# Kernel tuning notes

Measured on AMD Instinct MI355X. Metric: run time of the kernel, lower is better.

Reference implementation:

```python
import jax, jax.numpy as jnp
import numpy as np
from jax import lax

NB_DIGITS = 2
BASE = 10
NUMS = BASE ** NB_DIGITS            # 100 possible values per number
SUMS = 2 * (NUMS - 1) + 1           # 199 possible sums (circuit roots)
B = 4096                            # logical batch size
N_IMAGES = B * 2 * NB_DIGITS        # 16384 digit images


def setup_inputs() -> dict:
    key = jax.random.key(0)
    ks = jax.random.split(key, 11)
    s = 0.1
    return {
        "images": jax.random.normal(ks[0], (N_IMAGES, 1, 28, 28), jnp.float32),
        "conv1_w": jax.random.normal(ks[1], (6, 1, 5, 5), jnp.float32) * s,
        "conv1_b": jax.random.normal(ks[2], (6,), jnp.float32) * s,
        "conv2_w": jax.random.normal(ks[3], (16, 6, 5, 5), jnp.float32) * s,
        "conv2_b": jax.random.normal(ks[4], (16,), jnp.float32) * s,
        "fc1_w": jax.random.normal(ks[5], (120, 256), jnp.float32) * s,
        "fc1_b": jax.random.normal(ks[6], (120,), jnp.float32) * s,
        "fc2_w": jax.random.normal(ks[7], (84, 120), jnp.float32) * s,
        "fc2_b": jax.random.normal(ks[8], (84,), jnp.float32) * s,
        "fc3_w": jax.random.normal(ks[9], (10, 84), jnp.float32) * s,
        "fc3_b": jax.random.normal(ks[10], (10,), jnp.float32) * s,
    }


def _conv(x, w, b):
    y = lax.conv_general_dilated(x, w, (1, 1), 'VALID',
                                 dimension_numbers=('NCHW', 'OIHW', 'NCHW'))
    return y + b[None, :, None, None]


def _maxpool2(x):
    return lax.reduce_window(x, -jnp.inf, lax.max, (1, 1, 2, 2), (1, 1, 2, 2), 'VALID')


def _lenet(x, c1w, c1b, c2w, c2b, f1w, f1b, f2w, f2b, f3w, f3b):
    x = jax.nn.relu(_maxpool2(_conv(x, c1w, c1b)))   # [N,6,12,12]
    x = jax.nn.relu(_maxpool2(_conv(x, c2w, c2b)))   # [N,16,4,4]
    x = x.reshape(-1, 16 * 4 * 4)
    x = jax.nn.relu(x @ f1w.T + f1b)
    x = jax.nn.relu(x @ f2w.T + f2b)
    x = x @ f3w.T + f3b
    return jax.nn.log_softmax(x, axis=-1)            # [N,10]


def _circuit(lp):
    # lp: [B, 2*NB_DIGITS, 10] per-digit log-probs.
    # Vars layout from get_circuit: positions 0..NB_DIGITS-1 = n1 digits (MSB first),
    # positions NB_DIGITS..2*NB_DIGITS-1 = n2 digits. Neg-literal weights are 0 in
    # log space (the `zeros` arg), so each model's weight = sum of digit log-probs;
    # OR over models = logsumexp grouped by n1+n2.
    d = jnp.arange(NUMS)
    hi, lo = d // BASE, d % BASE
    lp1 = lp[:, 0, hi] + lp[:, 1, lo]                # [B, NUMS] log P(n1=k)
    lp2 = lp[:, 2, hi] + lp[:, 3, lo]                # [B, NUMS] log P(n2=k)
    M = (lp1[:, :, None] + lp2[:, None, :]).reshape(lp.shape[0], -1)  # [B, NUMS^2]
    seg = (jnp.arange(NUMS)[:, None] + jnp.arange(NUMS)[None, :]).reshape(-1)
    Mf = M.T                                          # [NUMS^2, B]
    m = jax.ops.segment_max(Mf, seg, num_segments=SUMS)              # [SUMS, B]
    ssum = jax.ops.segment_sum(jnp.exp(Mf - m[seg]), seg, num_segments=SUMS)
    return (jnp.log(ssum) + m).T                      # [B, SUMS] log P(sum=s)


def reference(images, conv1_w, conv1_b, conv2_w, conv2_b,
              fc1_w, fc1_b, fc2_w, fc2_b, fc3_w, fc3_b):
    logp = _lenet(images, conv1_w, conv1_b, conv2_w, conv2_b,
                  fc1_w, fc1_b, fc2_w, fc2_b, fc3_w, fc3_b)   # [N_IMAGES,10]
    lp = logp.reshape(B, 2 * NB_DIGITS, BASE)
    return _circuit(lp)
```

## Files before the change

kernel.cpp:

```cpp
#include <hip/hip_runtime.h>
#include <hip/hip_bf16.h>
#include <math.h>

#define SUMS 199
#define NBLK 1024

typedef __attribute__((ext_vector_type(8))) short short8;
typedef __attribute__((ext_vector_type(4))) float float4v;

union Frag8 { short8 v; unsigned u[4]; uint4 q; };

static __device__ inline unsigned pk_bf16(float a, float b) {
    __hip_bfloat162 h = __float22bfloat162_rn(make_float2(a, b));
    union { __hip_bfloat162 h; unsigned u; } c; c.h = h; return c.u;
}

__global__ __launch_bounds__(256) void convert_weights(
    const float* __restrict__ f1w, const float* __restrict__ f2w,
    const float* __restrict__ f3w, const float* __restrict__ c1w,
    const float* __restrict__ c2w, uint4* __restrict__ ws)
{
    const int g = blockIdx.x * 256 + threadIdx.x;
    if (g >= 6400) return;
    float v[8];
    if (g < 5824) {
        const float* W; int O, K, ld, nt, s, l;
        if (g < 4096)      { W = f1w; O = 120; K = 256; ld = 256; nt = g >> 9; s = (g >> 6) & 7; l = g & 63; }
        else if (g < 5632) { const int f = g - 4096; W = f2w; O = 84; K = 120; ld = 120; nt = f >> 8; s = (f >> 6) & 3; l = f & 63; }
        else               { const int f = g - 5632; W = f3w; O = 10; K = 84;  ld = 84;  nt = 0; s = f >> 6; l = f & 63; }
        const int o = nt * 16 + (l & 15);
        #pragma unroll
        for (int j = 0; j < 8; ++j) {
            const int k = 32 * s + 8 * (l >> 4) + j;
            v[j] = (o < O && k < K) ? W[o * ld + k] : 0.f;
        }
    } else if (g < 6336) {
        const int f = g - 5824, s = f >> 6, l = f & 63;
        const int c = l & 15, h = l >> 4;
        const int pos = 4 * s + h;
        const int ky = pos / 5, kx = pos % 5;
        const bool ok = (pos < 25);
        #pragma unroll
        for (int jp = 0; jp < 4; ++jp) {
            v[2 * jp]     = (ok && 2 * jp < 6)     ? c2w[c * 150 + (2 * jp) * 25 + ky * 5 + kx]     : 0.f;
            v[2 * jp + 1] = (ok && 2 * jp + 1 < 6) ? c2w[c * 150 + (2 * jp + 1) * 25 + ky * 5 + kx] : 0.f;
        }
    } else {
        const int l = (g - 6336) & 63;
        const int c = l & 15, h = l >> 4;
        const int oc = c >> 1, xs = c & 1;
        #pragma unroll
        for (int j = 0; j < 8; ++j) {
            const int p = h * 4 + (j >> 1);
            float w = 0.f;
            if (p < 15 && c < 12) {
                const int ky = p / 3, kx = 2 * (p % 3) + (j & 1) - xs;
                if (kx >= 0 && kx < 5) w = c1w[oc * 25 + ky * 5 + kx];
            }
            v[j] = w;
        }
    }
    uint4 r;
    r.x = pk_bf16(v[0], v[1]); r.y = pk_bf16(v[2], v[3]);
    r.z = pk_bf16(v[4], v[5]); r.w = pk_bf16(v[6], v[7]);
    ws[g] = r;
}

__global__ __launch_bounds__(256, 4) void lenet_circuit_kernel(
    const float* __restrict__ images,
    const float* __restrict__ c1b, const float* __restrict__ c2b,
    const float* __restrict__ f1b, const float* __restrict__ f2b,
    const float* __restrict__ f3b, const uint4* __restrict__ wsb,
    float* __restrict__ out)
{
    __shared__ __align__(16) unsigned char s_mem[39680];
    unsigned*       imgu = (unsigned*)s_mem;
    uint2*          imgw = (uint2*)s_mem;
    unsigned short* p1s  = (unsigned short*)(s_mem + 12672);
    const uint4*    p1u4 = (const uint4*)(s_mem + 12672);
    unsigned*       A1d  = (unsigned*)(s_mem + 31232);
    const uint4*    A1q  = (const uint4*)(s_mem + 31232);
    float*          pgf  = (float*)(s_mem + 7680);
    float*          Hf   = (float*)(s_mem + 8448);
    float*          Lf   = (float*)(s_mem + 8768);

    const int t = threadIdx.x, bid = blockIdx.x;
    const int lane = t & 63, wav = t >> 6;
    const int c = lane & 15, h = lane >> 4;
    const uint4 z4 = {0u, 0u, 0u, 0u};

    const int qxo = c >> 2, parity = (c >> 1) & 1, irel = c & 1;

    {
        uint4* pz = (uint4*)(s_mem + 12672) + 2 * wav * 145;
        for (int j = lane; j < 290; j += 64) pz[j] = z4;
    }
    Frag8 a1; a1.q = wsb[6336 + lane];
    Frag8 w2[7];
    #pragma unroll
    for (int s = 0; s < 7; ++s) w2[s].q = wsb[5824 + s * 64 + lane];
    int koff[7];
    #pragma unroll
    for (int s = 0; s < 7; ++s) {
        const int pos = 4 * s + h;
        koff[s] = (pos < 25) ? (pos / 5) * 12 + (pos % 5) : 0;
    }
    int pd[4];
    #pragma unroll
    for (int q = 0; q < 4; ++q) {
        const int p = 4 * h + q;
        pd[q] = (p < 15) ? (p / 3) * 14 + (p % 3) : 0;
    }
    float bias0 = 0.f, bias1 = 0.f;
    if (h < 3) { bias0 = c1b[2 * h]; bias1 = c1b[2 * h + 1]; }
    const float b2v = c2b[c];

    float4 pf[7];
    {
        const float4* g1 = (const float4*)(images + (size_t)bid * 12544 + 6272) + 392 * wav;
        #pragma unroll
        for (int k = 0; k < 7; ++k) {
            const int i = lane + 64 * k;
            if (i < 392) pf[k] = g1[i];
        }
    }

    auto do_stage1 = [&]() {
        #pragma unroll
        for (int k = 0; k < 7; ++k) {
            const int i = lane + 64 * k;
            if (i < 392) {
                const int im = 2 * wav + (i >= 196);
                const int j = i - ((i >= 196) ? 196 : 0);
                uint2 wv; wv.x = pk_bf16(pf[k].x, pf[k].y); wv.y = pk_bf16(pf[k].z, pf[k].w);
                imgw[im * 198 + j] = wv;
            }
        }
    };
    auto do_conv1 = [&]() {
        const int img = 2 * wav + irel;
        const int imb = img * 396 + parity * 14 + qxo;
        for (int qy = 0; qy < 12; ++qy) {
            #pragma unroll
            for (int qxg = 0; qxg < 3; ++qxg) {
                const int base = imb + qy * 28 + qxg * 4;
                Frag8 bf;
                #pragma unroll
                for (int q = 0; q < 4; ++q) bf.u[q] = imgu[base + pd[q]];
                float4v acc = {0.f, 0.f, 0.f, 0.f};
                acc = __builtin_amdgcn_mfma_f32_16x16x32_bf16(a1.v, bf.v, acc, 0, 0, 0);
                float v0 = fmaxf(acc[0], acc[1]);
                float v1 = fmaxf(acc[2], acc[3]);
                v0 = fmaxf(v0, __shfl_xor(v0, 2));
                v1 = fmaxf(v1, __shfl_xor(v1, 2));
                if (parity == 0 && h < 3) {
                    const int qx = qxg * 4 + qxo;
                    *(unsigned*)&p1s[img * 1160 + qy * 96 + qx * 8 + 2 * h] =
                        pk_bf16(fmaxf(v0 + bias0, 0.f), fmaxf(v1 + bias1, 0.f));
                }
            }
        }
    };
    auto do_conv2 = [&](int pass) {
        const int pxl = (c & 1) + 2 * ((c >> 2) & 1);
        const int pyl = ((c >> 1) & 1) + 2 * ((c >> 3) & 1);
        #pragma unroll
        for (int ii = 0; ii < 2; ++ii) {
            const int i0 = 2 * wav + ii;
            #pragma unroll
            for (int mt = 0; mt < 4; ++mt) {
                const int px = pxl + 4 * (mt & 1), py = pyl + 4 * (mt >> 1);
                const int base = i0 * 145 + py * 12 + px;
                float4v acc = {0.f, 0.f, 0.f, 0.f};
                #pragma unroll
                for (int s = 0; s < 7; ++s) {
                    Frag8 af; af.q = p1u4[base + koff[s]];
                    acc = __builtin_amdgcn_mfma_f32_16x16x32_bf16(af.v, w2[s].v, acc, 0, 0, 0);
                }
                const float p = fmaxf(fmaxf(acc[0], acc[1]), fmaxf(acc[2], acc[3]));
                float v = fmaxf(p + b2v, 0.f);
                const float vp = __shfl_xor(v, 16);
                if ((h & 1) == 0) {
                    const int qy = (h >> 1) + 2 * (mt >> 1);
                    A1d[(pass * 8 + i0) * 132 + c * 8 + qy * 2 + (mt & 1)] = pk_bf16(v, vp);
                }
            }
        }
    };

    {
        const float4* g = (const float4*)(images + (size_t)bid * 12544) + 392 * wav;
        #pragma unroll
        for (int k = 0; k < 7; ++k) {
            const int i = lane + 64 * k;
            if (i < 392) {
                const float4 v = g[i];
                const int im = 2 * wav + (i >= 196);
                const int j = i - ((i >= 196) ? 196 : 0);
                uint2 wv; wv.x = pk_bf16(v.x, v.y); wv.y = pk_bf16(v.z, v.w);
                imgw[im * 198 + j] = wv;
            }
        }
    }
    do_conv1();
    do_stage1();
    do_conv2(0);
    do_conv1();
    do_conv2(1);
    __syncthreads();

    {
        unsigned* A2d = (unsigned*)s_mem;
        if (t < 64) A2d[(t >> 2) * 68 + 60 + (t & 3)] = 0u;
        float4v acc0 = {0.f, 0.f, 0.f, 0.f}, acc1 = acc0;
        const int nt0 = 2 * wav;
        #pragma unroll
        for (int s = 0; s < 8; ++s) {
            Frag8 af; af.q = A1q[c * 33 + 4 * s + h];
            Frag8 b0; b0.q = wsb[(nt0 * 8 + s) * 64 + lane];
            Frag8 b1; b1.q = wsb[((nt0 + 1) * 8 + s) * 64 + lane];
            acc0 = __builtin_amdgcn_mfma_f32_16x16x32_bf16(af.v, b0.v, acc0, 0, 0, 0);
            acc1 = __builtin_amdgcn_mfma_f32_16x16x32_bf16(af.v, b1.v, acc1, 0, 0, 0);
        }
        #pragma unroll
        for (int ntl = 0; ntl < 2; ++ntl) {
            const int o = 32 * wav + 16 * ntl + c;
            const float bias = (o < 120) ? f1b[o] : 0.f;
            #pragma unroll
            for (int r = 0; r < 4; ++r) {
                float v = fmaxf((ntl ? acc1[r] : acc0[r]) + bias, 0.f);
                const float vp = __shfl_xor(v, 1);
                if ((c & 1) == 0 && o < 120)
                    A2d[(4 * h + r) * 68 + (o >> 1)] = pk_bf16(v, vp);
            }
        }
    }
    __syncthreads();

    {
        unsigned* A3d = (unsigned*)(s_mem + 4352);
        if (t < 96) A3d[(t / 6) * 52 + 42 + (t % 6)] = 0u;
        if (wav < 3) {
            const uint4* A2q = (const uint4*)s_mem;
            float4v acc0 = {0.f, 0.f, 0.f, 0.f}, acc1 = acc0;
            const int nt0 = 2 * wav;
            #pragma unroll
            for (int s = 0; s < 4; ++s) {
                Frag8 af; af.q = A2q[c * 17 + 4 * s + h];
                Frag8 b0; b0.q = wsb[4096 + (nt0 * 4 + s) * 64 + lane];
                Frag8 b1; b1.q = wsb[4096 + ((nt0 + 1) * 4 + s) * 64 + lane];
                acc0 = __builtin_amdgcn_mfma_f32_16x16x32_bf16(af.v, b0.v, acc0, 0, 0, 0);
                acc1 = __builtin_amdgcn_mfma_f32_16x16x32_bf16(af.v, b1.v, acc1, 0, 0, 0);
            }
            #pragma unroll
            for (int ntl = 0; ntl < 2; ++ntl) {
                const int o = 32 * wav + 16 * ntl + c;
                const float bias = (o < 84) ? f2b[o] : 0.f;
                #pragma unroll
                for (int r = 0; r < 4; ++r) {
                    float v = fmaxf((ntl ? acc1[r] : acc0[r]) + bias, 0.f);
                    const float vp = __shfl_xor(v, 1);
                    if ((c & 1) == 0 && o < 84)
                        A3d[(4 * h + r) * 52 + (o >> 1)] = pk_bf16(v, vp);
                }
            }
        }
    }
    __syncthreads();

    {
        const uint4* A3q = (const uint4*)(s_mem + 4352);
        float4v acc = {0.f, 0.f, 0.f, 0.f};
        #pragma unroll
        for (int s = 0; s < 3; ++s) {
            Frag8 af; af.q = A3q[c * 13 + 4 * s + h];
            Frag8 b; b.q = wsb[5632 + s * 64 + lane];
            acc = __builtin_amdgcn_mfma_f32_16x16x32_bf16(af.v, b.v, acc, 0, 0, 0);
        }
        const float bias = (c < 10) ? f3b[c] : 0.f;
        float x[4], m[4], e[4], sm[4];
        #pragma unroll
        for (int r = 0; r < 4; ++r) {
            x[r] = (c < 10) ? (acc[r] + bias) : -INFINITY;
            m[r] = x[r];
        }
        #pragma unroll
        for (int d = 1; d <= 8; d <<= 1)
            #pragma unroll
            for (int r = 0; r < 4; ++r) m[r] = fmaxf(m[r], __shfl_xor(m[r], d));
        #pragma unroll
        for (int r = 0; r < 4; ++r) { e[r] = (c < 10) ? expf(x[r] - m[r]) : 0.f; sm[r] = e[r]; }
        #pragma unroll
        for (int d = 1; d <= 8; d <<= 1)
            #pragma unroll
            for (int r = 0; r < 4; ++r) sm[r] += __shfl_xor(sm[r], d);
        if (c < 10 && h == wav) {
            #pragma unroll
            for (int r = 0; r < 4; ++r)
                pgf[(4 * wav + r) * 12 + c] = e[r] / sm[r];
        }

        if (lane < 38) {
            const int isH = (lane < 19), b = isH ? lane : lane - 19;
            const float* pg = pgf + 4 * wav * 12;
            const float* PA = pg + (isH ? 0 : 12);
            const float* PB = pg + (isH ? 24 : 36);
            const int ilo = (b > 9) ? b - 9 : 0;
            const int ihi = (b < 9) ? b : 9;
            float s = 0.f;
            for (int i = ilo; i <= ihi; ++i) s += PA[i] * PB[b - i];
            (isH ? Hf : Lf)[wav * 20 + b] = s;
        }

        const float* H = Hf + wav * 20;
        const float* L = Lf + wav * 20;
        for (int s = lane; s < SUMS; s += 64) {
            const int bmin = (s > 18) ? (s - 9) / 10 : 0;
            int bmax = s / 10; if (bmax > 18) bmax = 18;
            float sum = 0.f;
            for (int b = bmin; b <= bmax; ++b) sum += H[b] * L[s - 10 * b];
            out[((size_t)bid * 4 + wav) * SUMS + s] = logf(sum);
        }
    }
}

extern "C" void kernel_launch(void* const* d_in, const int* in_sizes, int n_in,
                              void* d_out, int out_size, void* d_ws, size_t ws_size,
                              hipStream_t stream) {
    const float* images = (const float*)d_in[0];
    const float* c1w = (const float*)d_in[1];
    const float* c1b = (const float*)d_in[2];
    const float* c2w = (const float*)d_in[3];
    const float* c2b = (const float*)d_in[4];
    const float* f1w = (const float*)d_in[5];
    const float* f1b = (const float*)d_in[6];
    const float* f2w = (const float*)d_in[7];
    const float* f2b = (const float*)d_in[8];
    const float* f3w = (const float*)d_in[9];
    const float* f3b = (const float*)d_in[10];
    float* out = (float*)d_out;

    convert_weights<<<25, 256, 0, stream>>>(f1w, f2w, f3w, c1w, c2w, (uint4*)d_ws);
    lenet_circuit_kernel<<<NBLK, 256, 0, stream>>>(
        images, c1b, c2b, f1b, f2b, f3b, (const uint4*)d_ws, out);
}
```

Before: 136.0 us.

## Halve per-block work to 8 images, doubling blocks and occupancy

Each block now handles 8 images (2 samples) instead of 16. This halves shared memory and raises the launch-bounds occupancy target from 4 to 8 blocks per CU. Conv1 is remapped so each wave processes one image per pass, and conv2 interleaves 4 independent MFMA chains while loading weights per step instead of keeping them in registers. The FC stages now use only 8 of the 16 MFMA rows, which wastes half the MFMA throughput in those stages. The software prefetch of the second image half is dropped, trading explicit overlap for more concurrent blocks.

After: 157.8 us. 1.16x slower.

```diff
diff --git a/kernel.cpp b/kernel.cpp
--- a/kernel.cpp
+++ b/kernel.cpp
@@ -3,7 +3,7 @@
 #include <math.h>
 
 #define SUMS 199
-#define NBLK 1024
+#define NBLK 2048
 
 typedef __attribute__((ext_vector_type(8))) short short8;
 typedef __attribute__((ext_vector_type(4))) float float4v;
@@ -66,39 +66,36 @@
     ws[g] = r;
 }
 
-__global__ __launch_bounds__(256, 4) void lenet_circuit_kernel(
+__global__ __launch_bounds__(256, 8) void lenet_circuit_kernel(
     const float* __restrict__ images,
     const float* __restrict__ c1b, const float* __restrict__ c2b,
     const float* __restrict__ f1b, const float* __restrict__ f2b,
     const float* __restrict__ f3b, const uint4* __restrict__ wsb,
     float* __restrict__ out)
 {
-    __shared__ __align__(16) unsigned char s_mem[39680];
+    __shared__ __align__(16) unsigned char s_mem[19840];
     unsigned*       imgu = (unsigned*)s_mem;
     uint2*          imgw = (uint2*)s_mem;
-    unsigned short* p1s  = (unsigned short*)(s_mem + 12672);
-    const uint4*    p1u4 = (const uint4*)(s_mem + 12672);
-    unsigned*       A1d  = (unsigned*)(s_mem + 31232);
-    const uint4*    A1q  = (const uint4*)(s_mem + 31232);
-    float*          pgf  = (float*)(s_mem + 7680);
-    float*          Hf   = (float*)(s_mem + 8448);
-    float*          Lf   = (float*)(s_mem + 8768);
+    unsigned short* p1s  = (unsigned short*)(s_mem + 6336);
+    const uint4*    p1u4 = (const uint4*)(s_mem + 6336);
+    unsigned*       A1d  = (unsigned*)(s_mem + 15616);
+    const uint4*    A1q  = (const uint4*)(s_mem + 15616);
+    float*          pgf  = (float*)(s_mem + 4352);
+    float*          Hf   = (float*)(s_mem + 4736);
+    float*          Lf   = (float*)(s_mem + 4896);
 
     const int t = threadIdx.x, bid = blockIdx.x;
     const int lane = t & 63, wav = t >> 6;
     const int c = lane & 15, h = lane >> 4;
     const uint4 z4 = {0u, 0u, 0u, 0u};
 
-    const int qxo = c >> 2, parity = (c >> 1) & 1, irel = c & 1;
+    const int qxo = c & 3, par = (c >> 2) & 1, qyo = c >> 3;
 
     {
-        uint4* pz = (uint4*)(s_mem + 12672) + 2 * wav * 145;
-        for (int j = lane; j < 290; j += 64) pz[j] = z4;
+        uint4* pz = (uint4*)(s_mem + 6336) + wav * 145;
+        for (int j = lane; j < 145; j += 64) pz[j] = z4;
     }
     Frag8 a1; a1.q = wsb[6336 + lane];
-    Frag8 w2[7];
-    #pragma unroll
-    for (int s = 0; s < 7; ++s) w2[s].q = wsb[5824 + s * 64 + lane];
     int koff[7];
     #pragma unroll
     for (int s = 0; s < 7; ++s) {
@@ -115,108 +112,86 @@
     if (h < 3) { bias0 = c1b[2 * h]; bias1 = c1b[2 * h + 1]; }
     const float b2v = c2b[c];
 
-    float4 pf[7];
-    {
-        const float4* g1 = (const float4*)(images + (size_t)bid * 12544 + 6272) + 392 * wav;
-        #pragma unroll
-        for (int k = 0; k < 7; ++k) {
-            const int i = lane + 64 * k;
-            if (i < 392) pf[k] = g1[i];
-        }
-    }
-
-    auto do_stage1 = [&]() {
-        #pragma unroll
-        for (int k = 0; k < 7; ++k) {
-            const int i = lane + 64 * k;
-            if (i < 392) {
-                const int im = 2 * wav + (i >= 196);
-                const int j = i - ((i >= 196) ? 196 : 0);
-                uint2 wv; wv.x = pk_bf16(pf[k].x, pf[k].y); wv.y = pk_bf16(pf[k].z, pf[k].w);
-                imgw[im * 198 + j] = wv;
-            }
-        }
-    };
-    auto do_conv1 = [&]() {
-        const int img = 2 * wav + irel;
-        const int imb = img * 396 + parity * 14 + qxo;
-        for (int qy = 0; qy < 12; ++qy) {
-            #pragma unroll
-            for (int qxg = 0; qxg < 3; ++qxg) {
-                const int base = imb + qy * 28 + qxg * 4;
-                Frag8 bf;
+    for (int pass = 0; pass < 2; ++pass) {
+        {
+            const float4* g = (const float4*)(images) +
+                              ((size_t)bid * 8 + pass * 4 + wav) * 196;
+            #pragma unroll
+            for (int k = 0; k < 4; ++k) {
+                const int i = lane + 64 * k;
+                if (i < 196) {
+                    const float4 v = g[i];
+                    uint2 wv; wv.x = pk_bf16(v.x, v.y); wv.y = pk_bf16(v.z, v.w);
+                    imgw[wav * 198 + i] = wv;
+                }
+            }
+        }
+        {
+            const int sbase = wav * 396 + (2 * qyo + par) * 14 + qxo;
+            for (int Q = 0; Q < 6; ++Q) {
                 #pragma unroll
-                for (int q = 0; q < 4; ++q) bf.u[q] = imgu[base + pd[q]];
-                float4v acc = {0.f, 0.f, 0.f, 0.f};
-                acc = __builtin_amdgcn_mfma_f32_16x16x32_bf16(a1.v, bf.v, acc, 0, 0, 0);
-                float v0 = fmaxf(acc[0], acc[1]);
-                float v1 = fmaxf(acc[2], acc[3]);
-                v0 = fmaxf(v0, __shfl_xor(v0, 2));
-                v1 = fmaxf(v1, __shfl_xor(v1, 2));
-                if (parity == 0 && h < 3) {
-                    const int qx = qxg * 4 + qxo;
-                    *(unsigned*)&p1s[img * 1160 + qy * 96 + qx * 8 + 2 * h] =
-                        pk_bf16(fmaxf(v0 + bias0, 0.f), fmaxf(v1 + bias1, 0.f));
-                }
-            }
-        }
-    };
-    auto do_conv2 = [&](int pass) {
-        const int pxl = (c & 1) + 2 * ((c >> 2) & 1);
-        const int pyl = ((c >> 1) & 1) + 2 * ((c >> 3) & 1);
-        #pragma unroll
-        for (int ii = 0; ii < 2; ++ii) {
-            const int i0 = 2 * wav + ii;
+                for (int qxg = 0; qxg < 3; ++qxg) {
+                    const int base = sbase + Q * 56 + qxg * 4;
+                    Frag8 bf;
+                    #pragma unroll
+                    for (int q = 0; q < 4; ++q) bf.u[q] = imgu[base + pd[q]];
+                    float4v acc = {0.f, 0.f, 0.f, 0.f};
+                    acc = __builtin_amdgcn_mfma_f32_16x16x32_bf16(a1.v, bf.v, acc, 0, 0, 0);
+                    float v0 = fmaxf(acc[0], acc[1]);
+                    float v1 = fmaxf(acc[2], acc[3]);
+                    v0 = fmaxf(v0, __shfl_xor(v0, 4));
+                    v1 = fmaxf(v1, __shfl_xor(v1, 4));
+                    if (par == 0 && h < 3) {
+                        const int qy = 2 * Q + qyo, qx = qxg * 4 + qxo;
+                        *(unsigned*)&p1s[wav * 1160 + qy * 96 + qx * 8 + 2 * h] =
+                            pk_bf16(fmaxf(v0 + bias0, 0.f), fmaxf(v1 + bias1, 0.f));
+                    }
+                }
+            }
+        }
+        {
+            const int pxl = (c & 1) + 2 * ((c >> 2) & 1);
+            const int pyl = ((c >> 1) & 1) + 2 * ((c >> 3) & 1);
+            int pbase[4];
+            #pragma unroll
+            for (int mt = 0; mt < 4; ++mt)
+                pbase[mt] = wav * 145 + (pyl + 4 * (mt >> 1)) * 12 + pxl + 4 * (mt & 1);
+            float4v acc[4];
+            #pragma unroll
+            for (int mt = 0; mt < 4; ++mt) acc[mt] = (float4v){0.f, 0.f, 0.f, 0.f};
+            #pragma unroll
+            for (int s = 0; s < 7; ++s) {
+                Frag8 wz; wz.q = wsb[5824 + s * 64 + lane];
+                #pragma unroll
+                for (int mt = 0; mt < 4; ++mt) {
+                    Frag8 af; af.q = p1u4[pbase[mt] + koff[s]];
+                    acc[mt] = __builtin_amdgcn_mfma_f32_16x16x32_bf16(af.v, wz.v, acc[mt], 0, 0, 0);
+                }
+            }
+            const int img = pass * 4 + wav;
             #pragma unroll
             for (int mt = 0; mt < 4; ++mt) {
-                const int px = pxl + 4 * (mt & 1), py = pyl + 4 * (mt >> 1);
-                const int base = i0 * 145 + py * 12 + px;
-                float4v acc = {0.f, 0.f, 0.f, 0.f};
-                #pragma unroll
-                for (int s = 0; s < 7; ++s) {
-                    Frag8 af; af.q = p1u4[base + koff[s]];
-                    acc = __builtin_amdgcn_mfma_f32_16x16x32_bf16(af.v, w2[s].v, acc, 0, 0, 0);
-                }
-                const float p = fmaxf(fmaxf(acc[0], acc[1]), fmaxf(acc[2], acc[3]));
+                const float p = fmaxf(fmaxf(acc[mt][0], acc[mt][1]),
+                                      fmaxf(acc[mt][2], acc[mt][3]));
                 float v = fmaxf(p + b2v, 0.f);
                 const float vp = __shfl_xor(v, 16);
                 if ((h & 1) == 0) {
                     const int qy = (h >> 1) + 2 * (mt >> 1);
-                    A1d[(pass * 8 + i0) * 132 + c * 8 + qy * 2 + (mt & 1)] = pk_bf16(v, vp);
-                }
-            }
-        }
-    };
-
-    {
-        const float4* g = (const float4*)(images + (size_t)bid * 12544) + 392 * wav;
-        #pragma unroll
-        for (int k = 0; k < 7; ++k) {
-            const int i = lane + 64 * k;
-            if (i < 392) {
-                const float4 v = g[i];
-                const int im = 2 * wav + (i >= 196);
-                const int j = i - ((i >= 196) ? 196 : 0);
-                uint2 wv; wv.x = pk_bf16(v.x, v.y); wv.y = pk_bf16(v.z, v.w);
-                imgw[im * 198 + j] = wv;
-            }
-        }
-    }
-    do_conv1();
-    do_stage1();
-    do_conv2(0);
-    do_conv1();
-    do_conv2(1);
+                    A1d[img * 132 + c * 8 + qy * 2 + (mt & 1)] = pk_bf16(v, vp);
+                }
+            }
+        }
+    }
     __syncthreads();
 
     {
         unsigned* A2d = (unsigned*)s_mem;
-        if (t < 64) A2d[(t >> 2) * 68 + 60 + (t & 3)] = 0u;
+        if (t < 32) A2d[(t >> 2) * 68 + 60 + (t & 3)] = 0u;
         float4v acc0 = {0.f, 0.f, 0.f, 0.f}, acc1 = acc0;
         const int nt0 = 2 * wav;
         #pragma unroll
         for (int s = 0; s < 8; ++s) {
-            Frag8 af; af.q = A1q[c * 33 + 4 * s + h];
+            Frag8 af; af.q = A1q[(c & 7) * 33 + 4 * s + h];
             Frag8 b0; b0.q = wsb[(nt0 * 8 + s) * 64 + lane];
             Frag8 b1; b1.q = wsb[((nt0 + 1) * 8 + s) * 64 + lane];
             acc0 = __builtin_amdgcn_mfma_f32_16x16x32_bf16(af.v, b0.v, acc0, 0, 0, 0);
@@ -230,7 +205,7 @@
             for (int r = 0; r < 4; ++r) {
                 float v = fmaxf((ntl ? acc1[r] : acc0[r]) + bias, 0.f);
                 const float vp = __shfl_xor(v, 1);
-                if ((c & 1) == 0 && o < 120)
+                if ((c & 1) == 0 && o < 120 && h < 2)
                     A2d[(4 * h + r) * 68 + (o >> 1)] = pk_bf16(v, vp);
             }
         }
@@ -238,15 +213,15 @@
     __syncthreads();
 
     {
-        unsigned* A3d = (unsigned*)(s_mem + 4352);
-        if (t < 96) A3d[(t / 6) * 52 + 42 + (t % 6)] = 0u;
+        unsigned* A3d = (unsigned*)(s_mem + 2560);
+        if (t < 48) A3d[(t / 6) * 52 + 42 + (t % 6)] = 0u;
         if (wav < 3) {
             const uint4* A2q = (const uint4*)s_mem;
             float4v acc0 = {0.f, 0.f, 0.f, 0.f}, acc1 = acc0;
             const int nt0 = 2 * wav;
             #pragma unroll
             for (int s = 0; s < 4; ++s) {
-                Frag8 af; af.q = A2q[c * 17 + 4 * s + h];
+                Frag8 af; af.q = A2q[(c & 7) * 17 + 4 * s + h];
                 Frag8 b0; b0.q = wsb[4096 + (nt0 * 4 + s) * 64 + lane];
                 Frag8 b1; b1.q = wsb[4096 + ((nt0 + 1) * 4 + s) * 64 + lane];
                 acc0 = __builtin_amdgcn_mfma_f32_16x16x32_bf16(af.v, b0.v, acc0, 0, 0, 0);
@@ -260,7 +235,7 @@
                 for (int r = 0; r < 4; ++r) {
                     float v = fmaxf((ntl ? acc1[r] : acc0[r]) + bias, 0.f);
                     const float vp = __shfl_xor(v, 1);
-                    if ((c & 1) == 0 && o < 84)
+                    if ((c & 1) == 0 && o < 84 && h < 2)
                         A3d[(4 * h + r) * 52 + (o >> 1)] = pk_bf16(v, vp);
                 }
             }
@@ -268,12 +243,12 @@
     }
     __syncthreads();
 
-    {
-        const uint4* A3q = (const uint4*)(s_mem + 4352);
+    if (wav < 2) {
+        const uint4* A3q = (const uint4*)(s_mem + 2560);
         float4v acc = {0.f, 0.f, 0.f, 0.f};
         #pragma unroll
         for (int s = 0; s < 3; ++s) {
-            Frag8 af; af.q = A3q[c * 13 + 4 * s + h];
+            Frag8 af; af.q = A3q[(c & 7) * 13 + 4 * s + h];
             Frag8 b; b.q = wsb[5632 + s * 64 + lane];
             acc = __builtin_amdgcn_mfma_f32_16x16x32_bf16(af.v, b.v, acc, 0, 0, 0);
         }
@@ -319,7 +294,7 @@
             int bmax = s / 10; if (bmax > 18) bmax = 18;
             float sum = 0.f;
             for (int b = bmin; b <= bmax; ++b) sum += H[b] * L[s - 10 * b];
-            out[((size_t)bid * 4 + wav) * SUMS + s] = logf(sum);
+            out[((size_t)bid * 2 + wav) * SUMS + s] = logf(sum);
         }
     }
 }
```
